# Kernel tuning notes

Measured on AMD Instinct MI355X. Metric: run time of the kernel, lower is better.

Reference implementation:

```python
import jax, jax.numpy as jnp
import numpy as np

B, L, D = 8, 4096, 256
H, C = 2, 128
DEG = 16  # incoming ring neighbors per node (excluding self loop)


def _build_edge_index():
    # Block-diagonal graph replicated per batch element, like _get_buffer.
    i = np.arange(L)
    offs = np.arange(1, DEG + 1)
    src_g = ((i[:, None] + offs[None, :]) % L).reshape(-1)   # [L*DEG]
    dst_g = np.repeat(i, DEG)                                 # [L*DEG]
    base = (np.arange(B) * L)[:, None]
    src = (src_g[None, :] + base).reshape(-1)
    dst = (dst_g[None, :] + base).reshape(-1)
    # PyG GATConv: remove_self_loops + add_self_loops -> exactly one self loop/node
    self_idx = np.arange(B * L)
    src = np.concatenate([src, self_idx])
    dst = np.concatenate([dst, self_idx])
    return jnp.asarray(np.stack([src, dst]), dtype=jnp.int32)  # [2, E]


def setup_inputs() -> dict:
    key = jax.random.key(0)
    k0, k1, k2, k3 = jax.random.split(key, 4)
    glorot = 1.0 / np.sqrt(D)
    return {
        "x": jax.random.normal(k0, (B, L, D), jnp.float32),
        "edge_index": _build_edge_index(),
        "W": jax.random.normal(k1, (D, H * C), jnp.float32) * glorot,
        "att_src": jax.random.normal(k2, (H, C), jnp.float32) * (1.0 / np.sqrt(C)),
        "att_dst": jax.random.normal(k3, (H, C), jnp.float32) * (1.0 / np.sqrt(C)),
        "bias": jnp.zeros((H * C,), jnp.float32),
    }


def reference(x, edge_index, W, att_src, att_dst, bias):
    b, l, d = x.shape
    n = b * l
    h_, c_ = att_src.shape
    xf = x.reshape(n, d)                                   # flatten batch of graphs
    res = xf
    h = (xf @ W).reshape(n, h_, c_)                        # [N,H,C] projected features
    a_src = jnp.einsum('nhc,hc->nh', h, att_src)           # per-node src logits
    a_dst = jnp.einsum('nhc,hc->nh', h, att_dst)
    s, t = edge_index[0], edge_index[1]
    alpha = jax.nn.leaky_relu(a_src[s] + a_dst[t], 0.2)    # [E,H]
    # softmax over incoming edges of each destination node
    amax = jax.ops.segment_max(alpha, t, num_segments=n)
    ex = jnp.exp(alpha - amax[t])
    denom = jax.ops.segment_sum(ex, t, num_segments=n)
    attn = ex / jnp.where(denom[t] > 0, denom[t], 1.0)     # [E,H]
    msg = h[s] * attn[:, :, None]                          # [E,H,C]
    out = jax.ops.segment_sum(msg, t, num_segments=n).reshape(n, h_ * c_) + bias
    out = jax.nn.relu(out) + res                           # relu + residual
    return out.reshape(b, l, h_ * c_)
```

## Files before the change

kernel.cpp:

```cpp
#include <hip/hip_runtime.h>

#define LL 4096
#define DD 256
#define TM 64
#define HALO 16
#define ROWS (TM + HALO)
#define NTH 512
#define APAD 40
#define HTS 104
#define WBS 104

typedef float f32x4 __attribute__((ext_vector_type(4)));
typedef __bf16 bf16x8 __attribute__((ext_vector_type(8)));
typedef unsigned short us8 __attribute__((ext_vector_type(8)));
typedef unsigned short us4 __attribute__((ext_vector_type(4)));

__device__ __forceinline__ unsigned short f2bf(float f) {
    union { float f; unsigned u; } v; v.f = f;
    unsigned r = v.u + 0x7fffu + ((v.u >> 16) & 1u);
    return (unsigned short)(r >> 16);
}

__global__ void prep_w(const float* __restrict__ W, unsigned short* __restrict__ Wt) {
    int t = blockIdx.x * blockDim.x + threadIdx.x;
    int l = t & 63;
    int kk = (t >> 6) & 7;
    int ct = t >> 9;
    int col = (ct << 4) + (l & 15);
    int kbase = kk * 32 + ((l >> 4) << 3);
    us8 v;
    for (int j = 0; j < 8; ++j) v[j] = f2bf(W[(kbase + j) * 256 + col]);
    *reinterpret_cast<us8*>(Wt + t * 8) = v;
}

__global__ __launch_bounds__(NTH, 4) void gat_fused(
    const float* __restrict__ x, const unsigned short* __restrict__ Wt,
    const float* __restrict__ att_src, const float* __restrict__ att_dst,
    const float* __restrict__ bias, float* __restrict__ out)
{
    __shared__ unsigned short h_t[256][HTS];
    __shared__ float alog[ROWS][2][2];
    __shared__ __align__(16) unsigned char smem_u[2 * 64 * WBS * 2];
    unsigned short (*a_lds)[APAD] = reinterpret_cast<unsigned short(*)[APAD]>(smem_u);
    unsigned short (*wband)[WBS]  = reinterpret_cast<unsigned short(*)[WBS]>(smem_u);

    const int tid  = threadIdx.x;
    const int lane = tid & 63;
    const int wv   = tid >> 6;
    const int lo   = lane & 15;
    const int hi   = lane >> 4;
    const int blk  = blockIdx.x;
    const int batch = blk >> 6;
    const int i0    = (blk & 63) * TM;
    const long xbase = (long)batch * (LL * DD);
    const int ct0 = wv * 2;
    const int hd  = wv >> 2;

    {
        int chan = tid >> 1, half = tid & 1;
        us8 z = {0, 0, 0, 0, 0, 0, 0, 0};
        *reinterpret_cast<us8*>(&h_t[chan][80 + half * 8]) = z;
        if (tid < 320) ((float*)alog)[tid] = 0.f;
    }

    f32x4 acc[5][2];
    for (int a = 0; a < 5; ++a)
        for (int b = 0; b < 2; ++b)
            acc[a][b] = (f32x4){0.f, 0.f, 0.f, 0.f};

    for (int kk = 0; kk < 8; ++kk) {
        __syncthreads();
        for (int lin = tid; lin < 640; lin += NTH) {
            int r  = lin >> 3;
            int kq = (lin & 7) << 2;
            int grow = (i0 + r) & (LL - 1);
            const float4 v = *reinterpret_cast<const float4*>(
                x + xbase + (long)grow * DD + kk * 32 + kq);
            us4 p;
            p[0] = f2bf(v.x); p[1] = f2bf(v.y); p[2] = f2bf(v.z); p[3] = f2bf(v.w);
            *reinterpret_cast<us4*>(&a_lds[r][kq]) = p;
        }
        __syncthreads();

        bf16x8 bfrag[2];
        for (int c = 0; c < 2; ++c) {
            us8 raw = *reinterpret_cast<const us8*>(
                Wt + (size_t)((((ct0 + c) * 8 + kk) * 64 + lane) * 8));
            bfrag[c] = __builtin_bit_cast(bf16x8, raw);
        }
        for (int rt = 0; rt < 5; ++rt) {
            us8 araw = *reinterpret_cast<const us8*>(&a_lds[rt * 16 + lo][hi * 8]);
            bf16x8 afrag = __builtin_bit_cast(bf16x8, araw);
            acc[rt][0] = __builtin_amdgcn_mfma_f32_16x16x32_bf16(bfrag[0], afrag, acc[rt][0], 0, 0, 0);
            acc[rt][1] = __builtin_amdgcn_mfma_f32_16x16x32_bf16(bfrag[1], afrag, acc[rt][1], 0, 0, 0);
        }
    }

    {
        const float4 as0 = *reinterpret_cast<const float4*>(att_src + ct0 * 16 + hi * 4);
        const float4 as1 = *reinterpret_cast<const float4*>(att_src + (ct0 + 1) * 16 + hi * 4);
        const float4 ad0 = *reinterpret_cast<const float4*>(att_dst + ct0 * 16 + hi * 4);
        const float4 ad1 = *reinterpret_cast<const float4*>(att_dst + (ct0 + 1) * 16 + hi * 4);

        float ps[5], pd[5];
        for (int rt = 0; rt < 5; ++rt) {
            f32x4 a0 = acc[rt][0], a1 = acc[rt][1];
            ps[rt] = a0[0] * as0.x + a0[1] * as0.y + a0[2] * as0.z + a0[3] * as0.w
                   + a1[0] * as1.x + a1[1] * as1.y + a1[2] * as1.z + a1[3] * as1.w;
            pd[rt] = a0[0] * ad0.x + a0[1] * ad0.y + a0[2] * ad0.z + a0[3] * ad0.w
                   + a1[0] * ad1.x + a1[1] * ad1.y + a1[2] * ad1.z + a1[3] * ad1.w;
            int xrow = rt * 16 + lo;
            for (int j = 0; j < 4; ++j)
                h_t[ct0 * 16 + hi * 4 + j][xrow] = f2bf(a0[j]);
            for (int j = 0; j < 4; ++j)
                h_t[(ct0 + 1) * 16 + hi * 4 + j][xrow] = f2bf(a1[j]);
        }
        for (int rt = 0; rt < 5; ++rt) {
            ps[rt] += __shfl_xor(ps[rt], 16);
            ps[rt] += __shfl_xor(ps[rt], 32);
            pd[rt] += __shfl_xor(pd[rt], 16);
            pd[rt] += __shfl_xor(pd[rt], 32);
        }
        if (hi == 0) {
            for (int rt = 0; rt < 5; ++rt) {
                atomicAdd(&alog[rt * 16 + lo][hd][0], ps[rt]);
                atomicAdd(&alog[rt * 16 + lo][hd][1], pd[rt]);
            }
        }
    }

    float4 res[4][2];
    for (int rt = 0; rt < 4; ++rt)
        for (int c = 0; c < 2; ++c)
            res[rt][c] = *reinterpret_cast<const float4*>(
                x + xbase + (long)(i0 + rt * 16 + lo) * DD + (ct0 + c) * 16 + hi * 4);

    __syncthreads();

    if (tid < 128) {
        int r = tid >> 1, h2 = tid & 1;
        unsigned short* wrow = &wband[h2 * 64 + r][0];
        us8 z = {0, 0, 0, 0, 0, 0, 0, 0};
        for (int q = 0; q < 13; ++q) *reinterpret_cast<us8*>(wrow + q * 8) = z;
        float ad = alog[r][h2][1];
        float al[17];
        float mx = -1e30f;
        for (int k = 0; k < 17; ++k) {
            float s = (k < 16) ? alog[r + 1 + k][h2][0] : alog[r][h2][0];
            float v = s + ad;
            v = (v > 0.f) ? v : 0.2f * v;
            al[k] = v;
            mx = fmaxf(mx, v);
        }
        float sum = 0.f;
        for (int k = 0; k < 17; ++k) { al[k] = __expf(al[k] - mx); sum += al[k]; }
        float inv = 1.f / sum;
        wrow[r] = f2bf(al[16] * inv);
        for (int k = 0; k < 16; ++k) wrow[r + 1 + k] = f2bf(al[k] * inv);
    }
    __syncthreads();

    {
        f32x4 acc2[4][2];
        for (int a = 0; a < 4; ++a)
            for (int b = 0; b < 2; ++b)
                acc2[a][b] = (f32x4){0.f, 0.f, 0.f, 0.f};

        for (int kq = 0; kq < 3; ++kq) {
            bf16x8 bfr[4];
            for (int rt = 0; rt < 4; ++rt) {
                us8 raw = *reinterpret_cast<const us8*>(
                    &wband[hd * 64 + rt * 16 + lo][kq * 32 + hi * 8]);
                bfr[rt] = __builtin_bit_cast(bf16x8, raw);
            }
            for (int c = 0; c < 2; ++c) {
                us8 araw = *reinterpret_cast<const us8*>(
                    &h_t[(ct0 + c) * 16 + lo][kq * 32 + hi * 8]);
                bf16x8 afr = __builtin_bit_cast(bf16x8, araw);
                for (int rt = 0; rt < 4; ++rt)
                    acc2[rt][c] = __builtin_amdgcn_mfma_f32_16x16x32_bf16(afr, bfr[rt], acc2[rt][c], 0, 0, 0);
            }
        }

        const float4 b40 = *reinterpret_cast<const float4*>(bias + ct0 * 16 + hi * 4);
        const float4 b41 = *reinterpret_cast<const float4*>(bias + (ct0 + 1) * 16 + hi * 4);
        for (int rt = 0; rt < 4; ++rt)
            for (int c = 0; c < 2; ++c) {
                const float4 b4 = c ? b41 : b40;
                f32x4 s = acc2[rt][c];
                long g = xbase + (long)(i0 + rt * 16 + lo) * DD + (ct0 + c) * 16 + hi * 4;
                float4 o;
                o.x = fmaxf(s[0] + b4.x, 0.f) + res[rt][c].x;
                o.y = fmaxf(s[1] + b4.y, 0.f) + res[rt][c].y;
                o.z = fmaxf(s[2] + b4.z, 0.f) + res[rt][c].z;
                o.w = fmaxf(s[3] + b4.w, 0.f) + res[rt][c].w;
                *reinterpret_cast<float4*>(out + g) = o;
            }
    }
}

extern "C" void kernel_launch(void* const* d_in, const int* in_sizes, int n_in,
                              void* d_out, int out_size, void* d_ws, size_t ws_size,
                              hipStream_t stream) {
    const float* x       = (const float*)d_in[0];
    const float* W       = (const float*)d_in[2];
    const float* att_src = (const float*)d_in[3];
    const float* att_dst = (const float*)d_in[4];
    const float* bias    = (const float*)d_in[5];
    float* out           = (float*)d_out;
    unsigned short* Wt   = (unsigned short*)d_ws;

    hipLaunchKernelGGL(prep_w, dim3(32), dim3(256), 0, stream, W, Wt);
    hipLaunchKernelGGL(gat_fused, dim3(512), dim3(NTH), 0, stream,
                       x, Wt, att_src, att_dst, bias, out);
}
```

Baseline: 35.36 us.

## Double-buffer x tile staging and prefetch next K-slice into registers

```diff
diff --git a/kernel.cpp b/kernel.cpp
--- a/kernel.cpp
+++ b/kernel.cpp
@@ -9,6 +9,7 @@
 #define APAD 40
 #define HTS 104
 #define WBS 104
+#define ABUF_BYTES (ROWS * APAD * 2)
 
 typedef float f32x4 __attribute__((ext_vector_type(4)));
 typedef __bf16 bf16x8 __attribute__((ext_vector_type(8)));
@@ -41,7 +42,8 @@
     __shared__ unsigned short h_t[256][HTS];
     __shared__ float alog[ROWS][2][2];
     __shared__ __align__(16) unsigned char smem_u[2 * 64 * WBS * 2];
-    unsigned short (*a_lds)[APAD] = reinterpret_cast<unsigned short(*)[APAD]>(smem_u);
+    unsigned short (*abuf0)[APAD] = reinterpret_cast<unsigned short(*)[APAD]>(smem_u);
+    unsigned short (*abuf1)[APAD] = reinterpret_cast<unsigned short(*)[APAD]>(smem_u + ABUF_BYTES);
     unsigned short (*wband)[WBS]  = reinterpret_cast<unsigned short(*)[WBS]>(smem_u);
 
     const int tid  = threadIdx.x;
@@ -68,31 +70,63 @@
         for (int b = 0; b < 2; ++b)
             acc[a][b] = (f32x4){0.f, 0.f, 0.f, 0.f};
 
+    const int s0r = tid >> 3, s0k = (tid & 7) << 2;
+    const int s1r = (tid + 512) >> 3, s1k = ((tid + 512) & 7) << 2;
+    const float* xrow0 = x + xbase + (long)((i0 + s0r) & (LL - 1)) * DD + s0k;
+    const float* xrow1 = x + xbase + (long)((i0 + s1r) & (LL - 1)) * DD + s1k;
+    const unsigned short* wtb0 = Wt + (size_t)(ct0 * 8 * 64 + lane) * 8;
+    const unsigned short* wtb1 = Wt + (size_t)((ct0 + 1) * 8 * 64 + lane) * 8;
+
+    float4 cur0, cur1, nxt0, nxt1;
+    us8 braw0, braw1, nbraw0, nbraw1;
+
+    cur0 = *reinterpret_cast<const float4*>(xrow0);
+    if (tid < 128) cur1 = *reinterpret_cast<const float4*>(xrow1);
+    braw0 = *reinterpret_cast<const us8*>(wtb0);
+    braw1 = *reinterpret_cast<const us8*>(wtb1);
+    {
+        us4 p;
+        p[0] = f2bf(cur0.x); p[1] = f2bf(cur0.y); p[2] = f2bf(cur0.z); p[3] = f2bf(cur0.w);
+        *reinterpret_cast<us4*>(&abuf0[s0r][s0k]) = p;
+        if (tid < 128) {
+            us4 q;
+            q[0] = f2bf(cur1.x); q[1] = f2bf(cur1.y); q[2] = f2bf(cur1.z); q[3] = f2bf(cur1.w);
+            *reinterpret_cast<us4*>(&abuf0[s1r][s1k]) = q;
+        }
+    }
+
+#pragma unroll
     for (int kk = 0; kk < 8; ++kk) {
+        unsigned short (*buf)[APAD]  = (kk & 1) ? abuf1 : abuf0;
+        unsigned short (*nbuf)[APAD] = (kk & 1) ? abuf0 : abuf1;
+        if (kk < 7) {
+            nxt0 = *reinterpret_cast<const float4*>(xrow0 + (kk + 1) * 32);
+            if (tid < 128) nxt1 = *reinterpret_cast<const float4*>(xrow1 + (kk + 1) * 32);
+            nbraw0 = *reinterpret_cast<const us8*>(wtb0 + (size_t)(kk + 1) * 64 * 8);
+            nbraw1 = *reinterpret_cast<const us8*>(wtb1 + (size_t)(kk + 1) * 64 * 8);
+        }
         __syncthreads();
-        for (int lin = tid; lin < 640; lin += NTH) {
-            int r  = lin >> 3;
-            int kq = (lin & 7) << 2;
-            int grow = (i0 + r) & (LL - 1);
-            const float4 v = *reinterpret_cast<const float4*>(
-                x + xbase + (long)grow * DD + kk * 32 + kq);
+
+        bf16x8 bfrag0 = __builtin_bit_cast(bf16x8, braw0);
+        bf16x8 bfrag1 = __builtin_bit_cast(bf16x8, braw1);
+        for (int rt = 0; rt < 5; ++rt) {
+            us8 araw = *reinterpret_cast<const us8*>(&buf[rt * 16 + lo][hi * 8]);
+            bf16x8 afrag = __builtin_bit_cast(bf16x8, araw);
+            acc[rt][0] = __builtin_amdgcn_mfma_f32_16x16x32_bf16(bfrag0, afrag, acc[rt][0], 0, 0, 0);
+            acc[rt][1] = __builtin_amdgcn_mfma_f32_16x16x32_bf16(bfrag1, afrag, acc[rt][1], 0, 0, 0);
+        }
+
+        if (kk < 7) {
             us4 p;
-            p[0] = f2bf(v.x); p[1] = f2bf(v.y); p[2] = f2bf(v.z); p[3] = f2bf(v.w);
-            *reinterpret_cast<us4*>(&a_lds[r][kq]) = p;
-        }
-        __syncthreads();
-
-        bf16x8 bfrag[2];
-        for (int c = 0; c < 2; ++c) {
-            us8 raw = *reinterpret_cast<const us8*>(
-                Wt + (size_t)((((ct0 + c) * 8 + kk) * 64 + lane) * 8));
-            bfrag[c] = __builtin_bit_cast(bf16x8, raw);
-        }
-        for (int rt = 0; rt < 5; ++rt) {
-            us8 araw = *reinterpret_cast<const us8*>(&a_lds[rt * 16 + lo][hi * 8]);
-            bf16x8 afrag = __builtin_bit_cast(bf16x8, araw);
-            acc[rt][0] = __builtin_amdgcn_mfma_f32_16x16x32_bf16(bfrag[0], afrag, acc[rt][0], 0, 0, 0);
-            acc[rt][1] = __builtin_amdgcn_mfma_f32_16x16x32_bf16(bfrag[1], afrag, acc[rt][1], 0, 0, 0);
+            p[0] = f2bf(nxt0.x); p[1] = f2bf(nxt0.y); p[2] = f2bf(nxt0.z); p[3] = f2bf(nxt0.w);
+            *reinterpret_cast<us4*>(&nbuf[s0r][s0k]) = p;
+            if (tid < 128) {
+                us4 q;
+                q[0] = f2bf(nxt1.x); q[1] = f2bf(nxt1.y); q[2] = f2bf(nxt1.z); q[3] = f2bf(nxt1.w);
+                *reinterpret_cast<us4*>(&nbuf[s1r][s1k]) = q;
+            }
+            braw0 = nbraw0;
+            braw1 = nbraw1;
         }
     }
 
```

Result: faster. 32.52 us (-8.0%).
